# Kernel optimization log

Measured on AMD Instinct MI355X. Metric: run time of the kernel, lower is better.

## Reference

```python
import jax, jax.numpy as jnp
import numpy as np


def setup_inputs() -> dict:
    key = jax.random.key(0)
    ks = jax.random.split(key, 9)
    B, T, L, H2, E, V, OOV = 32, 48, 400, 512, 128, 50000, 100
    sd = lambda k, shape, s: jax.random.normal(k, shape, jnp.float32) * s
    return {
        "dec_hiddens": sd(ks[0], (B, T, H2), 1.0),   # decoder hidden state per step (B,T,2H)
        "enc_hiddens": sd(ks[1], (B, L, H2), 1.0),   # encoder outputs (B,L,2H)
        "W_enc": sd(ks[2], (H2, H2), 0.002),          # encoder-attention bilinear
        "W_dec": sd(ks[3], (H2, H2), 0.002),          # intra-decoder-attention bilinear
        "W_proj": sd(ks[4], (3 * H2, E), 0.02),       # decode2proj (6H -> emb)
        "W_vocab": sd(ks[5], (E, V), 0.05),           # proj2vocab (emb -> V, tied to embedding)
        "w_ptr": sd(ks[6], (3 * H2,), 0.02),          # ptr_gen weight
        "b_ptr": jnp.zeros((1,), jnp.float32),        # ptr_gen bias
        "extend_vocab": jax.random.randint(ks[7], (B, L), 0, V + OOV),
        "num_oov": OOV,
    }


def reference(dec_hiddens, enc_hiddens, W_enc, W_dec, W_proj, W_vocab,
              w_ptr, b_ptr, extend_vocab, num_oov):
    B, T, H2 = dec_hiddens.shape
    L = enc_hiddens.shape[1]
    V = W_vocab.shape[1]
    Vext = V + num_oov  # static python int
    rows = jnp.arange(B)[:, None]
    steps = jnp.arange(T)
    dec_seq = jnp.swapaxes(dec_hiddens, 0, 1)  # (T,B,2H) for scan

    def step(acc_exp, xs):
        h, t = xs  # h: (B,2H), t: scalar step index
        # intra-temporal encoder attention: exp(e) / running sum of previous exp(e)
        e = jnp.einsum('bh,hk,blk->bl', h, W_enc, enc_hiddens)  # (B,L)
        exp_e = jnp.exp(e)
        denom = jnp.where(t == 0, jnp.ones_like(acc_exp), acc_exp)
        temporal = exp_e / denom
        enc_att = temporal / temporal.sum(-1, keepdims=True)     # (B,L)
        enc_ctx = jnp.einsum('bl,blh->bh', enc_att, enc_hiddens)
        # intra-decoder attention over previous decoder hiddens (zeros at t=0)
        s = jnp.einsum('bh,hk,btk->bt', h, W_dec, dec_hiddens)   # (B,T)
        s = jnp.where((steps < t)[None, :], s, -1e30)
        datt = jax.nn.softmax(s, axis=-1)
        dec_ctx = jnp.where(t == 0, 0.0,
                            jnp.einsum('bt,bth->bh', datt, dec_hiddens))
        cat = jnp.concatenate([h, enc_ctx, dec_ctx], axis=-1)    # (B,6H)
        p = jax.nn.sigmoid(cat @ w_ptr + b_ptr)[:, None]         # (B,1) copy gate
        vocab_dist = jax.nn.softmax((cat @ W_proj) @ W_vocab, axis=-1)  # (B,V)
        # extended-vocab distribution: write softmax slice, scatter_add pointer dist
        final = jnp.zeros((B, Vext), dec_hiddens.dtype)
        final = final.at[:, :V].set((1.0 - p) * vocab_dist)
        final = final.at[rows, extend_vocab].add(p * enc_att)
        return acc_exp + exp_e, final

    init = jnp.zeros((B, L), dec_hiddens.dtype)
    _, out = jax.lax.scan(step, init, (dec_seq, steps))
    return jnp.swapaxes(out, 0, 1)  # (B,T,V+OOV)
```

## Files before the change

### kernel.cpp

```cpp
#include <hip/hip_runtime.h>
#include <hip/hip_bf16.h>
#include <cstdint>

typedef __attribute__((ext_vector_type(8))) short short8;
typedef __attribute__((ext_vector_type(4))) float floatx4;
typedef __attribute__((ext_vector_type(16))) float floatx16;

#define Bdim 32
#define Tdim 48
#define Ldim 400
#define Hdim 512
#define Edim 128
#define Vdim 50000
#define VEdim 50100
#define BTdim 1536
#define CATdim 1536
#define NPAD 50048
#define MTILES 96
#define NPART 782
#define NPSTRIDE 800

__device__ __forceinline__ short f2bf(float x){
    __hip_bfloat16 h = __float2bfloat16(x);
    union { __hip_bfloat16 h; short s; } u; u.h = h; return u.s;
}

__device__ __forceinline__ void gemm_nn_body(
    const float* __restrict__ A, int lda,
    const float* __restrict__ B, int ldb,
    float* __restrict__ C, int ldc,
    int M, int N, int K, int m0, int n0)
{
    __shared__ float As[16][68];
    __shared__ float Bs[16][68];
    const int tid = threadIdx.x;
    const int tx = tid & 15, ty = tid >> 4;
    const int ar = tid >> 2, ac = (tid & 3) * 4;
    const int br = tid >> 4, bc = (tid & 15) * 4;
    float acc[4][4] = {};
    float4 va = make_float4(0.f,0.f,0.f,0.f);
    float4 vb = make_float4(0.f,0.f,0.f,0.f);
    if (m0 + ar < M) va = *(const float4*)(A + (size_t)(m0+ar)*lda + ac);
    if (n0 + bc < N) vb = *(const float4*)(B + (size_t)br*ldb + n0 + bc);
    for (int k0 = 0; k0 < K; k0 += 16){
        As[ac+0][ar]=va.x; As[ac+1][ar]=va.y; As[ac+2][ar]=va.z; As[ac+3][ar]=va.w;
        Bs[br][bc+0]=vb.x; Bs[br][bc+1]=vb.y; Bs[br][bc+2]=vb.z; Bs[br][bc+3]=vb.w;
        __syncthreads();
        const int kn = k0 + 16;
        if (kn < K){
            va = make_float4(0.f,0.f,0.f,0.f);
            vb = make_float4(0.f,0.f,0.f,0.f);
            if (m0 + ar < M) va = *(const float4*)(A + (size_t)(m0+ar)*lda + kn + ac);
            if (n0 + bc < N) vb = *(const float4*)(B + (size_t)(kn+br)*ldb + n0 + bc);
        }
        #pragma unroll
        for (int k=0;k<16;k++){
            float a[4], b[4];
            #pragma unroll
            for (int i=0;i<4;i++) a[i] = As[k][ty*4+i];
            #pragma unroll
            for (int j=0;j<4;j++) b[j] = Bs[k][tx*4+j];
            #pragma unroll
            for (int i=0;i<4;i++)
                #pragma unroll
                for (int j=0;j<4;j++)
                    acc[i][j] += a[i]*b[j];
        }
        __syncthreads();
    }
    #pragma unroll
    for (int i=0;i<4;i++){
        int m = m0 + ty*4 + i;
        if (m >= M) continue;
        #pragma unroll
        for (int j=0;j<4;j++){
            int n = n0 + tx*4 + j;
            if (n < N) C[(size_t)m*ldc + n] = acc[i][j];
        }
    }
}

__device__ __forceinline__ void gemm_nt_body(
    const float* __restrict__ A, int lda,
    const float* __restrict__ B, int ldb,
    float* __restrict__ C, int ldc,
    int M, int N, int K, int m0, int n0)
{
    __shared__ float As[16][68];
    __shared__ float Bs[16][68];
    const int tid = threadIdx.x;
    const int tx = tid & 15, ty = tid >> 4;
    const int r = tid >> 2, c = (tid & 3) * 4;
    float acc[4][4] = {};
    float4 va = make_float4(0.f,0.f,0.f,0.f);
    float4 vb = make_float4(0.f,0.f,0.f,0.f);
    if (m0 + r < M) va = *(const float4*)(A + (size_t)(m0+r)*lda + c);
    if (n0 + r < N) vb = *(const float4*)(B + (size_t)(n0+r)*ldb + c);
    for (int k0 = 0; k0 < K; k0 += 16){
        As[c+0][r]=va.x; As[c+1][r]=va.y; As[c+2][r]=va.z; As[c+3][r]=va.w;
        Bs[c+0][r]=vb.x; Bs[c+1][r]=vb.y; Bs[c+2][r]=vb.z; Bs[c+3][r]=vb.w;
        __syncthreads();
        const int kn = k0 + 16;
        if (kn < K){
            va = make_float4(0.f,0.f,0.f,0.f);
            vb = make_float4(0.f,0.f,0.f,0.f);
            if (m0 + r < M) va = *(const float4*)(A + (size_t)(m0+r)*lda + kn + c);
            if (n0 + r < N) vb = *(const float4*)(B + (size_t)(n0+r)*ldb + kn + c);
        }
        #pragma unroll
        for (int k=0;k<16;k++){
            float a[4], b[4];
            #pragma unroll
            for (int i=0;i<4;i++) a[i] = As[k][ty*4+i];
            #pragma unroll
            for (int j=0;j<4;j++) b[j] = Bs[k][tx*4+j];
            #pragma unroll
            for (int i=0;i<4;i++)
                #pragma unroll
                for (int j=0;j<4;j++)
                    acc[i][j] += a[i]*b[j];
        }
        __syncthreads();
    }
    #pragma unroll
    for (int i=0;i<4;i++){
        int m = m0 + ty*4 + i;
        if (m >= M) continue;
        #pragma unroll
        for (int j=0;j<4;j++){
            int n = n0 + tx*4 + j;
            if (n < N) C[(size_t)m*ldc + n] = acc[i][j];
        }
    }
}

__global__ __launch_bounds__(256) void k_p12(
    const float* __restrict__ dec, const float* __restrict__ Wenc,
    const float* __restrict__ Wdec, float* __restrict__ P1, float* __restrict__ P2)
{
    const float* B = blockIdx.z ? Wdec : Wenc;
    float* C = blockIdx.z ? P2 : P1;
    gemm_nn_body(dec, Hdim, B, Hdim, C, Hdim, BTdim, Hdim, Hdim,
                 blockIdx.y*64, blockIdx.x*64);
}

__global__ __launch_bounds__(256) void k_es(
    const float* __restrict__ P1, const float* __restrict__ P2,
    const float* __restrict__ enc, const float* __restrict__ dec,
    float* __restrict__ ebuf, float* __restrict__ sbuf)
{
    int z = blockIdx.z;
    if (z < 32){
        gemm_nt_body(P1 + (size_t)z*Tdim*Hdim, Hdim,
                     enc + (size_t)z*Ldim*Hdim, Hdim,
                     ebuf + (size_t)z*Tdim*Ldim, Ldim,
                     Tdim, Ldim, Hdim, 0, blockIdx.x*64);
    } else {
        if (blockIdx.x) return;
        z -= 32;
        gemm_nt_body(P2 + (size_t)z*Tdim*Hdim, Hdim,
                     dec + (size_t)z*Tdim*Hdim, Hdim,
                     sbuf + (size_t)z*Tdim*Tdim, Tdim,
                     Tdim, Tdim, Hdim, 0, 0);
    }
}

__global__ __launch_bounds__(256) void k_tempdec(
    const float* __restrict__ e, float* __restrict__ att, float* __restrict__ sbuf)
{
    int bid = blockIdx.x;
    if (bid < 50){
        int idx = bid*256 + threadIdx.x;
        if (idx >= Bdim * Ldim) return;
        int b = idx / Ldim, l = idx % Ldim;
        const float* ep = e + (size_t)b * Tdim * Ldim + l;
        float* ap = att + (size_t)b * Tdim * Ldim + l;
        float acc = 0.f;
        for (int t = 0; t < Tdim; ++t){
            float x = __expf(ep[(size_t)t * Ldim]);
            float d = (t == 0) ? 1.f : acc;
            ap[(size_t)t * Ldim] = x / d;
            acc += x;
        }
    } else {
        int b = bid - 50;
        int t = threadIdx.x;
        if (t >= Tdim) return;
        float* row = sbuf + (size_t)b * Tdim * Tdim + (size_t)t * Tdim;
        if (t == 0){
            for (int j = 0; j < Tdim; ++j) row[j] = 0.f;
            return;
        }
        float mx = -1e30f;
        for (int j = 0; j < t; ++j) mx = fmaxf(mx, row[j]);
        float sum = 0.f;
        for (int j = 0; j < t; ++j){ float ex = __expf(row[j]-mx); row[j]=ex; sum+=ex; }
        float inv = 1.f/sum;
        for (int j = 0; j < t; ++j) row[j] *= inv;
        for (int j = t; j < Tdim; ++j) row[j] = 0.f;
    }
}

__global__ __launch_bounds__(256) void k_attnorm(float* __restrict__ att){
    int row = blockIdx.x;
    float* ap = att + (size_t)row * Ldim;
    float s = 0.f;
    for (int i = threadIdx.x; i < Ldim; i += 256) s += ap[i];
    #pragma unroll
    for (int off = 32; off; off >>= 1) s += __shfl_down(s, off, 64);
    __shared__ float red[4];
    if ((threadIdx.x & 63) == 0) red[threadIdx.x >> 6] = s;
    __syncthreads();
    float inv = 1.f / (red[0] + red[1] + red[2] + red[3]);
    for (int i = threadIdx.x; i < Ldim; i += 256) ap[i] *= inv;
}

__global__ __launch_bounds__(256) void k_ctx(
    const float* __restrict__ att, const float* __restrict__ sbuf,
    const float* __restrict__ enc, const float* __restrict__ dec,
    float* __restrict__ cat)
{
    int z = blockIdx.z;
    if (z >= 64){
        int idx = ((z-64)*8 + blockIdx.x)*256 + threadIdx.x;
        int m = idx >> 7, j = (idx & 127) << 2;
        *(float4*)(cat + (size_t)m*CATdim + j) =
            *(const float4*)(dec + (size_t)m*Hdim + j);
        return;
    }
    const float *A, *Bm; float* C; int lda, K;
    if (z < 32){
        A = att + (size_t)z*Tdim*Ldim; lda = Ldim;
        Bm = enc + (size_t)z*Ldim*Hdim;
        C = cat + (size_t)z*Tdim*CATdim + Hdim;
        K = Ldim;
    } else {
        int b = z - 32;
        A = sbuf + (size_t)b*Tdim*Tdim; lda = Tdim;
        Bm = dec + (size_t)b*Tdim*Hdim;
        C = cat + (size_t)b*Tdim*CATdim + 2*Hdim;
        K = Tdim;
    }
    gemm_nn_body(A, lda, Bm, Hdim, C, CATdim, Tdim, Hdim, K, 0, blockIdx.x*64);
}

__global__ __launch_bounds__(256) void k_proj(
    const float* __restrict__ cat, const float* __restrict__ Wproj,
    float* __restrict__ projf4)
{
    int z = blockIdx.z;
    gemm_nn_body(cat + (size_t)z*384, CATdim,
                 Wproj + (size_t)z*384*Edim, Edim,
                 projf4 + (size_t)z*BTdim*Edim, Edim,
                 BTdim, Edim, 384, blockIdx.y*64, blockIdx.x*64);
}

__global__ __launch_bounds__(256) void k_post(
    const float* __restrict__ cat, const float* __restrict__ wp,
    const float* __restrict__ bp, float* __restrict__ pg,
    const float* __restrict__ pf, short* __restrict__ pb,
    const float* __restrict__ Wv, short* __restrict__ Wt)
{
    __shared__ float smem[32*33];
    int bid = blockIdx.x;
    if (bid < BTdim){
        const float* cp = cat + (size_t)bid*CATdim;
        float s = 0.f;
        for (int i=threadIdx.x;i<CATdim;i+=256) s += cp[i]*wp[i];
        #pragma unroll
        for (int off=32; off; off>>=1) s += __shfl_down(s, off, 64);
        if ((threadIdx.x&63)==0) smem[threadIdx.x>>6]=s;
        __syncthreads();
        if (threadIdx.x==0){
            float tot = smem[0]+smem[1]+smem[2]+smem[3] + bp[0];
            pg[bid] = 1.f/(1.f + __expf(-tot));
        }
        return;
    }
    if (bid < BTdim + 768){
        int i = (bid - BTdim)*256 + threadIdx.x;
        pb[i] = f2bf(pf[i] + pf[i + 196608] + pf[i + 2*196608] + pf[i + 3*196608]);
        return;
    }
    int b2 = bid - (BTdim + 768);
    int n0 = (b2 % 1564)*32, k0 = (b2 / 1564)*32;
    float (*tile)[33] = reinterpret_cast<float(*)[33]>(smem);
    int x = threadIdx.x & 31, y0 = threadIdx.x >> 5;
    for (int yy=y0; yy<32; yy+=8){
        int n = n0 + x;
        tile[yy][x] = (n < Vdim) ? Wv[(size_t)(k0+yy)*Vdim + n] : 0.f;
    }
    __syncthreads();
    for (int yy=y0; yy<32; yy+=8){
        int n = n0 + yy;
        if (n < NPAD) Wt[(size_t)n*Edim + k0 + x] = f2bf(tile[x][yy]);
    }
}

__global__ __launch_bounds__(256) void k_logits1(
    const short* __restrict__ Ab, const short* __restrict__ Bt,
    float* __restrict__ partial)
{
    const int lane = threadIdx.x & 63;
    const int wave = threadIdx.x >> 6;
    const int l15 = lane & 15, quad = lane >> 4;
    const int wid = blockIdx.x*4 + wave;
    if (wid >= NPART) return;
    const int n0 = wid*64;
    short8 bfrag[4][4];
    #pragma unroll
    for (int ct=0;ct<4;ct++){
        const short* bp = Bt + (size_t)(n0 + ct*16 + l15)*Edim + quad*8;
        #pragma unroll
        for (int kk=0;kk<4;kk++) bfrag[ct][kk] = *(const short8*)(bp + kk*32);
    }
    float vmask[4];
    #pragma unroll
    for (int ct=0;ct<4;ct++) vmask[ct] = (n0 + ct*16 < Vdim) ? 1.f : 0.f;

    auto loadA = [&](int mt, short8 (&af)[4]){
        const short* ap = Ab + (size_t)(mt*16 + l15)*Edim + quad*8;
        #pragma unroll
        for (int kk=0;kk<4;kk++) af[kk] = *(const short8*)(ap + kk*32);
    };
    auto compute = [&](int mt, short8 (&af)[4]){
        floatx4 a0 = {0.f,0.f,0.f,0.f};
        floatx4 a1 = a0, a2 = a0, a3 = a0;
        #pragma unroll
        for (int kk=0;kk<4;kk++){
            a0 = __builtin_amdgcn_mfma_f32_16x16x32_bf16(bfrag[0][kk], af[kk], a0, 0, 0, 0);
            a1 = __builtin_amdgcn_mfma_f32_16x16x32_bf16(bfrag[1][kk], af[kk], a1, 0, 0, 0);
            a2 = __builtin_amdgcn_mfma_f32_16x16x32_bf16(bfrag[2][kk], af[kk], a2, 0, 0, 0);
            a3 = __builtin_amdgcn_mfma_f32_16x16x32_bf16(bfrag[3][kk], af[kk], a3, 0, 0, 0);
        }
        float s = vmask[0]*(__expf(a0[0])+__expf(a0[1])+__expf(a0[2])+__expf(a0[3]))
                + vmask[1]*(__expf(a1[0])+__expf(a1[1])+__expf(a1[2])+__expf(a1[3]))
                + vmask[2]*(__expf(a2[0])+__expf(a2[1])+__expf(a2[2])+__expf(a2[3]))
                + vmask[3]*(__expf(a3[0])+__expf(a3[1])+__expf(a3[2])+__expf(a3[3]));
        s += __shfl_xor(s, 16, 64);
        s += __shfl_xor(s, 32, 64);
        if (lane < 16)
            partial[(size_t)(mt*16 + l15)*NPSTRIDE + wid] = s;
    };

    short8 afA[4], afB[4];
    loadA(0, afA);
    for (int mt=0; mt<MTILES; mt+=2){
        loadA(mt+1, afB);
        compute(mt, afA);
        if (mt+2 < MTILES) loadA(mt+2, afA);
        compute(mt+1, afB);
    }
}

__global__ __launch_bounds__(256) void k_reduce(const float* __restrict__ partial,
                         const float* __restrict__ pg, float* __restrict__ scale){
    int m = blockIdx.x;
    float s = 0.f;
    for (int w = threadIdx.x; w < NPART; w += 256)
        s += partial[(size_t)m*NPSTRIDE + w];
    #pragma unroll
    for (int off=32; off; off>>=1) s += __shfl_down(s, off, 64);
    __shared__ float red[4];
    if ((threadIdx.x&63)==0) red[threadIdx.x>>6]=s;
    __syncthreads();
    if (threadIdx.x==0)
        scale[m] = (1.f - pg[m]) / (red[0]+red[1]+red[2]+red[3]);
}

__global__ __launch_bounds__(256) void k_logits2(
    const short* __restrict__ Ab, const short* __restrict__ Bt,
    const float* __restrict__ scale, float* __restrict__ out)
{
    const int lane = threadIdx.x & 63;
    const int wave = threadIdx.x >> 6;
    const int l31 = lane & 31, half = lane >> 5;
    const int n0 = blockIdx.x*128 + wave*32;
    const int n = n0 + l31;
    const int mt0 = blockIdx.y * 24;
    if (n0 >= Vdim){
        if (n < VEdim){
            for (int mt=mt0; mt<mt0+24; ++mt){
                #pragma unroll
                for (int r=0;r<16;r++){
                    int m = mt*32 + (r&3) + 8*(r>>2) + 4*half;
                    out[(size_t)m*VEdim + n] = 0.f;
                }
            }
        }
        return;
    }
    short8 bfrag[8];
    const short* bp = Bt + (size_t)n*Edim + half*8;
    #pragma unroll
    for (int kk=0;kk<8;kk++) bfrag[kk] = *(const short8*)(bp + kk*16);
    const bool valid = n < Vdim;
    for (int mt=mt0; mt<mt0+24; ++mt){
        floatx16 acc;
        #pragma unroll
        for (int i=0;i<16;i++) acc[i] = 0.f;
        const short* ap = Ab + (size_t)(mt*32 + l31)*Edim + half*8;
        #pragma unroll
        for (int kk=0;kk<8;kk++){
            short8 af = *(const short8*)(ap + kk*16);
            acc = __builtin_amdgcn_mfma_f32_32x32x16_bf16(af, bfrag[kk], acc, 0, 0, 0);
        }
        #pragma unroll
        for (int r=0;r<16;r++){
            int m = mt*32 + (r&3) + 8*(r>>2) + 4*half;
            if (valid) out[(size_t)m*VEdim + n] = scale[m]*__expf(acc[r]);
            else if (n < VEdim) out[(size_t)m*VEdim + n] = 0.f;
        }
    }
}

__global__ void k_scatter(const float* __restrict__ att, const float* __restrict__ pg,
                          const int* __restrict__ ev, float* __restrict__ out){
    int idx = blockIdx.x*256 + threadIdx.x;
    if (idx >= BTdim*Ldim) return;
    int m = idx / Ldim, l = idx % Ldim;
    int b = m / Tdim;
    int v = ev[b*Ldim + l];
    atomicAdd(&out[(size_t)m*VEdim + v], pg[m]*att[idx]);
}

extern "C" void kernel_launch(void* const* d_in, const int* in_sizes, int n_in,
                              void* d_out, int out_size, void* d_ws, size_t ws_size,
                              hipStream_t stream)
{
    const float* dec  = (const float*)d_in[0];
    const float* enc  = (const float*)d_in[1];
    const float* Wenc = (const float*)d_in[2];
    const float* Wdec = (const float*)d_in[3];
    const float* Wproj= (const float*)d_in[4];
    const float* Wvoc = (const float*)d_in[5];
    const float* wptr = (const float*)d_in[6];
    const float* bptr = (const float*)d_in[7];
    const int*   ev   = (const int*)d_in[8];
    float* out = (float*)d_out;

    float* ws = (float*)d_ws;
    float* P1      = ws;
    float* P2      = P1 + 786432;
    float* ebuf    = P2 + 786432;
    float* att     = ebuf + 614400;
    float* sbuf    = att + 614400;
    float* cat     = sbuf + 73728;
    float* projf4  = cat + 2359296;
    float* pg      = projf4 + 4*196608;
    float* scale   = pg + 1536;
    float* partial = scale + 1536;
    short* projb   = (short*)(partial + (size_t)BTdim*NPSTRIDE);
    short* Wt      = projb + 196608;

    dim3 blk(256);
    k_p12<<<dim3(8,24,2), blk, 0, stream>>>(dec, Wenc, Wdec, P1, P2);
    k_es<<<dim3(7,1,64), blk, 0, stream>>>(P1, P2, enc, dec, ebuf, sbuf);
    k_tempdec<<<dim3(82), blk, 0, stream>>>(ebuf, att, sbuf);
    k_attnorm<<<dim3(BTdim), blk, 0, stream>>>(att);
    k_ctx<<<dim3(8,1,160), blk, 0, stream>>>(att, sbuf, enc, dec, cat);
    k_proj<<<dim3(2,24,4), blk, 0, stream>>>(cat, Wproj, projf4);
    k_post<<<dim3(BTdim + 768 + 6256), blk, 0, stream>>>(cat, wptr, bptr, pg,
                                                         projf4, projb, Wvoc, Wt);
    k_logits1<<<dim3(196), blk, 0, stream>>>(projb, Wt, partial);
    k_reduce<<<dim3(BTdim), blk, 0, stream>>>(partial, pg, scale);
    k_logits2<<<dim3(392,2), blk, 0, stream>>>(projb, Wt, scale, out);
    k_scatter<<<dim3((BTdim*Ldim+255)/256), blk, 0, stream>>>(att, pg, ev, out);
}
```

Measured before the change: 704.4 us.

## Fuse pipeline into seven kernels with algebraic pointer gate and fused scatter

Collapses eleven launches into seven. The P1/P2 GEMMs, the W_vocab transpose, the cat copy and the precomputed enc/dec dot products with w_ptr all go into one grid. The pointer gate is now computed algebraically from attention-weighted projections (att·(enc·w2)) instead of a full dot over cat, and temporal attention, its normalisation and the decoder softmax are fused into one per-batch kernel. The projection GEMM runs K=1536 without split-K and writes bf16 directly. The logits partial sums go through atomics instead of a separate reduce kernel. The scatter is folded into the logits-write kernel by bucketing hits per column block. The trade-offs are less parallelism in the kE projection (48 blocks) and kC (32 blocks), plus a large LDS footprint in kC.

```diff
diff --git a/kernel.cpp b/kernel.cpp
--- a/kernel.cpp
+++ b/kernel.cpp
@@ -18,21 +18,26 @@
 #define NPAD 50048
 #define MTILES 96
 #define NPART 782
-#define NPSTRIDE 800
 
 __device__ __forceinline__ short f2bf(float x){
     __hip_bfloat16 h = __float2bfloat16(x);
     union { __hip_bfloat16 h; short s; } u; u.h = h; return u.s;
 }
 
+__device__ __forceinline__ float wred(float s){
+    #pragma unroll
+    for (int off = 32; off; off >>= 1) s += __shfl_xor(s, off, 64);
+    return s;
+}
+
+template<bool BF16>
 __device__ __forceinline__ void gemm_nn_body(
     const float* __restrict__ A, int lda,
     const float* __restrict__ B, int ldb,
-    float* __restrict__ C, int ldc,
-    int M, int N, int K, int m0, int n0)
-{
-    __shared__ float As[16][68];
-    __shared__ float Bs[16][68];
+    float* __restrict__ C, short* __restrict__ Cb, int ldc,
+    int M, int N, int K, int m0, int n0,
+    float (*As)[68], float (*Bs)[68])
+{
     const int tid = threadIdx.x;
     const int tx = tid & 15, ty = tid >> 4;
     const int ar = tid >> 2, ac = (tid & 3) * 4;
@@ -75,7 +80,10 @@
         #pragma unroll
         for (int j=0;j<4;j++){
             int n = n0 + tx*4 + j;
-            if (n < N) C[(size_t)m*ldc + n] = acc[i][j];
+            if (n < N){
+                if (BF16) Cb[(size_t)m*ldc + n] = f2bf(acc[i][j]);
+                else      C[(size_t)m*ldc + n]  = acc[i][j];
+            }
         }
     }
 }
@@ -84,10 +92,9 @@
     const float* __restrict__ A, int lda,
     const float* __restrict__ B, int ldb,
     float* __restrict__ C, int ldc,
-    int M, int N, int K, int m0, int n0)
-{
-    __shared__ float As[16][68];
-    __shared__ float Bs[16][68];
+    int M, int N, int K, int m0, int n0,
+    float (*As)[68], float (*Bs)[68])
+{
     const int tid = threadIdx.x;
     const int tx = tid & 15, ty = tid >> 4;
     const int r = tid >> 2, c = (tid & 3) * 4;
@@ -134,172 +141,209 @@
     }
 }
 
-__global__ __launch_bounds__(256) void k_p12(
+__global__ __launch_bounds__(256) void kA(
     const float* __restrict__ dec, const float* __restrict__ Wenc,
-    const float* __restrict__ Wdec, float* __restrict__ P1, float* __restrict__ P2)
-{
-    const float* B = blockIdx.z ? Wdec : Wenc;
-    float* C = blockIdx.z ? P2 : P1;
-    gemm_nn_body(dec, Hdim, B, Hdim, C, Hdim, BTdim, Hdim, Hdim,
-                 blockIdx.y*64, blockIdx.x*64);
-}
-
-__global__ __launch_bounds__(256) void k_es(
-    const float* __restrict__ P1, const float* __restrict__ P2,
-    const float* __restrict__ enc, const float* __restrict__ dec,
-    float* __restrict__ ebuf, float* __restrict__ sbuf)
-{
-    int z = blockIdx.z;
-    if (z < 32){
-        gemm_nt_body(P1 + (size_t)z*Tdim*Hdim, Hdim,
-                     enc + (size_t)z*Ldim*Hdim, Hdim,
-                     ebuf + (size_t)z*Tdim*Ldim, Ldim,
-                     Tdim, Ldim, Hdim, 0, blockIdx.x*64);
-    } else {
-        if (blockIdx.x) return;
-        z -= 32;
-        gemm_nt_body(P2 + (size_t)z*Tdim*Hdim, Hdim,
-                     dec + (size_t)z*Tdim*Hdim, Hdim,
-                     sbuf + (size_t)z*Tdim*Tdim, Tdim,
-                     Tdim, Tdim, Hdim, 0, 0);
-    }
-}
-
-__global__ __launch_bounds__(256) void k_tempdec(
-    const float* __restrict__ e, float* __restrict__ att, float* __restrict__ sbuf)
-{
+    const float* __restrict__ Wdec, float* __restrict__ P1, float* __restrict__ P2,
+    float* __restrict__ cat,
+    const float* __restrict__ Wv, short* __restrict__ Wt,
+    const float* __restrict__ enc, const float* __restrict__ wptr,
+    float* __restrict__ q_enc, float* __restrict__ q_dec,
+    float* __restrict__ sums)
+{
+    __shared__ float As[16][68];
+    __shared__ float Bs[16][68];
     int bid = blockIdx.x;
-    if (bid < 50){
+    if (bid < 384){
+        int z = bid / 192, r = bid % 192;
+        gemm_nn_body<false>(dec, Hdim, z ? Wdec : Wenc, Hdim,
+                            z ? P2 : P1, nullptr, Hdim,
+                            BTdim, Hdim, Hdim, (r>>3)*64, (r&7)*64, As, Bs);
+        return;
+    }
+    bid -= 384;
+    if (bid < 768){
         int idx = bid*256 + threadIdx.x;
-        if (idx >= Bdim * Ldim) return;
-        int b = idx / Ldim, l = idx % Ldim;
-        const float* ep = e + (size_t)b * Tdim * Ldim + l;
-        float* ap = att + (size_t)b * Tdim * Ldim + l;
-        float acc = 0.f;
-        for (int t = 0; t < Tdim; ++t){
-            float x = __expf(ep[(size_t)t * Ldim]);
-            float d = (t == 0) ? 1.f : acc;
-            ap[(size_t)t * Ldim] = x / d;
-            acc += x;
-        }
-    } else {
-        int b = bid - 50;
-        int t = threadIdx.x;
-        if (t >= Tdim) return;
-        float* row = sbuf + (size_t)b * Tdim * Tdim + (size_t)t * Tdim;
-        if (t == 0){
-            for (int j = 0; j < Tdim; ++j) row[j] = 0.f;
-            return;
-        }
-        float mx = -1e30f;
-        for (int j = 0; j < t; ++j) mx = fmaxf(mx, row[j]);
-        float sum = 0.f;
-        for (int j = 0; j < t; ++j){ float ex = __expf(row[j]-mx); row[j]=ex; sum+=ex; }
-        float inv = 1.f/sum;
-        for (int j = 0; j < t; ++j) row[j] *= inv;
-        for (int j = t; j < Tdim; ++j) row[j] = 0.f;
-    }
-}
-
-__global__ __launch_bounds__(256) void k_attnorm(float* __restrict__ att){
-    int row = blockIdx.x;
-    float* ap = att + (size_t)row * Ldim;
-    float s = 0.f;
-    for (int i = threadIdx.x; i < Ldim; i += 256) s += ap[i];
-    #pragma unroll
-    for (int off = 32; off; off >>= 1) s += __shfl_down(s, off, 64);
-    __shared__ float red[4];
-    if ((threadIdx.x & 63) == 0) red[threadIdx.x >> 6] = s;
-    __syncthreads();
-    float inv = 1.f / (red[0] + red[1] + red[2] + red[3]);
-    for (int i = threadIdx.x; i < Ldim; i += 256) ap[i] *= inv;
-}
-
-__global__ __launch_bounds__(256) void k_ctx(
-    const float* __restrict__ att, const float* __restrict__ sbuf,
-    const float* __restrict__ enc, const float* __restrict__ dec,
-    float* __restrict__ cat)
-{
-    int z = blockIdx.z;
-    if (z >= 64){
-        int idx = ((z-64)*8 + blockIdx.x)*256 + threadIdx.x;
         int m = idx >> 7, j = (idx & 127) << 2;
         *(float4*)(cat + (size_t)m*CATdim + j) =
             *(const float4*)(dec + (size_t)m*Hdim + j);
         return;
     }
-    const float *A, *Bm; float* C; int lda, K;
-    if (z < 32){
-        A = att + (size_t)z*Tdim*Ldim; lda = Ldim;
-        Bm = enc + (size_t)z*Ldim*Hdim;
-        C = cat + (size_t)z*Tdim*CATdim + Hdim;
-        K = Ldim;
+    bid -= 768;
+    if (bid < 6256){
+        float (*tile)[33] = reinterpret_cast<float(*)[33]>(&As[0][0]);
+        int n0 = (bid % 1564)*32, k0 = (bid / 1564)*32;
+        int x = threadIdx.x & 31, y0 = threadIdx.x >> 5;
+        for (int yy=y0; yy<32; yy+=8){
+            int n = n0 + x;
+            tile[yy][x] = (n < Vdim) ? Wv[(size_t)(k0+yy)*Vdim + n] : 0.f;
+        }
+        __syncthreads();
+        for (int yy=y0; yy<32; yy+=8){
+            int n = n0 + yy;
+            if (n < NPAD) Wt[(size_t)n*Edim + k0 + x] = f2bf(tile[x][yy]);
+        }
+        return;
+    }
+    bid -= 6256;
+    if (bid < 128){
+        int b = bid >> 2, part = bid & 3;
+        int wv = threadIdx.x >> 6, lane = threadIdx.x & 63;
+        const float* w2 = wptr + Hdim;
+        const float* w3 = wptr + 2*Hdim;
+        for (int r = part*100 + wv; r < part*100 + 100; r += 4){
+            const float* rp = enc + ((size_t)b*Ldim + r)*Hdim;
+            float s = 0.f;
+            #pragma unroll
+            for (int i = 0; i < 8; i++) s += rp[lane + i*64]*w2[lane + i*64];
+            s = wred(s);
+            if (lane == 0) q_enc[b*Ldim + r] = s;
+        }
+        if (part == 0){
+            for (int r = wv; r < Tdim; r += 4){
+                const float* rp = dec + ((size_t)b*Tdim + r)*Hdim;
+                float s = 0.f;
+                #pragma unroll
+                for (int i = 0; i < 8; i++) s += rp[lane + i*64]*w3[lane + i*64];
+                s = wred(s);
+                if (lane == 0) q_dec[b*Tdim + r] = s;
+            }
+        }
+        return;
+    }
+    for (int i = threadIdx.x; i < BTdim; i += 256) sums[i] = 0.f;
+}
+
+__global__ __launch_bounds__(256) void kB(
+    const float* __restrict__ P1, const float* __restrict__ P2,
+    const float* __restrict__ enc, const float* __restrict__ dec,
+    float* __restrict__ ebuf, float* __restrict__ sbuf)
+{
+    __shared__ float As[16][68];
+    __shared__ float Bs[16][68];
+    int bid = blockIdx.x;
+    if (bid < 224){
+        int z = bid / 7, x = bid % 7;
+        gemm_nt_body(P1 + (size_t)z*Tdim*Hdim, Hdim,
+                     enc + (size_t)z*Ldim*Hdim, Hdim,
+                     ebuf + (size_t)z*Tdim*Ldim, Ldim,
+                     Tdim, Ldim, Hdim, 0, x*64, As, Bs);
     } else {
-        int b = z - 32;
-        A = sbuf + (size_t)b*Tdim*Tdim; lda = Tdim;
-        Bm = dec + (size_t)b*Tdim*Hdim;
-        C = cat + (size_t)b*Tdim*CATdim + 2*Hdim;
-        K = Tdim;
-    }
-    gemm_nn_body(A, lda, Bm, Hdim, C, CATdim, Tdim, Hdim, K, 0, blockIdx.x*64);
-}
-
-__global__ __launch_bounds__(256) void k_proj(
+        int z = bid - 224;
+        gemm_nt_body(P2 + (size_t)z*Tdim*Hdim, Hdim,
+                     dec + (size_t)z*Tdim*Hdim, Hdim,
+                     sbuf + (size_t)z*Tdim*Tdim, Tdim,
+                     Tdim, Tdim, Hdim, 0, 0, As, Bs);
+    }
+}
+
+__global__ __launch_bounds__(512) void kC(
+    const float* __restrict__ e, float* __restrict__ att, float* __restrict__ sbuf,
+    const float* __restrict__ dec, const float* __restrict__ wptr,
+    const float* __restrict__ bptr,
+    const float* __restrict__ q_enc, const float* __restrict__ q_dec,
+    float* __restrict__ pg)
+{
+    __shared__ float att_s[Tdim][Ldim];
+    __shared__ float dE[Tdim], dD[Tdim], dH[Tdim];
+    const int b = blockIdx.x;
+    const int tid = threadIdx.x;
+    if (tid < Ldim){
+        const float* ep = e + (size_t)b*Tdim*Ldim + tid;
+        float acc = 0.f;
+        for (int t = 0; t < Tdim; ++t){
+            float x = __expf(ep[t*Ldim]);
+            att_s[t][tid] = x / (t ? acc : 1.f);
+            acc += x;
+        }
+    }
+    __syncthreads();
+    const int wv = tid >> 6, lane = tid & 63;
+    for (int t = wv; t < Tdim; t += 8){
+        float s1 = 0.f, s2 = 0.f;
+        for (int l = lane; l < Ldim; l += 64){
+            float a = att_s[t][l];
+            s1 += a;
+            s2 += a * q_enc[b*Ldim + l];
+        }
+        s1 = wred(s1); s2 = wred(s2);
+        float inv = 1.f/s1;
+        if (lane == 0) dE[t] = s2*inv;
+        for (int l = lane; l < Ldim; l += 64)
+            att[(size_t)(b*Tdim + t)*Ldim + l] = att_s[t][l]*inv;
+    }
+    for (int t = wv; t < Tdim; t += 8){
+        const float* hp = dec + ((size_t)b*Tdim + t)*Hdim;
+        float s = 0.f;
+        #pragma unroll
+        for (int i = 0; i < 8; i++) s += hp[lane + i*64]*wptr[lane + i*64];
+        s = wred(s);
+        if (lane == 0) dH[t] = s;
+    }
+    for (int t = wv; t < Tdim; t += 8){
+        float* row = sbuf + ((size_t)b*Tdim + t)*Tdim;
+        if (t == 0){
+            if (lane < Tdim) row[lane] = 0.f;
+            if (lane == 0) dD[0] = 0.f;
+        } else {
+            float v = (lane < t) ? row[lane] : -1e30f;
+            float mx = v;
+            #pragma unroll
+            for (int off = 32; off; off >>= 1) mx = fmaxf(mx, __shfl_xor(mx, off, 64));
+            float ex = (lane < t) ? __expf(v - mx) : 0.f;
+            float sm = wred(ex);
+            float nv = ex / sm;
+            if (lane < Tdim) row[lane] = nv;
+            float d = (lane < Tdim) ? nv * q_dec[b*Tdim + lane] : 0.f;
+            d = wred(d);
+            if (lane == 0) dD[t] = d;
+        }
+    }
+    __syncthreads();
+    if (tid < Tdim){
+        float tot = dH[tid] + dE[tid] + dD[tid] + bptr[0];
+        pg[b*Tdim + tid] = 1.f/(1.f + __expf(-tot));
+    }
+}
+
+__global__ __launch_bounds__(256) void kD(
+    const float* __restrict__ att, const float* __restrict__ sbuf,
+    const float* __restrict__ enc, const float* __restrict__ dec,
+    float* __restrict__ cat)
+{
+    __shared__ float As[16][68];
+    __shared__ float Bs[16][68];
+    int bid = blockIdx.x;
+    if (bid < 256){
+        int z = bid >> 3, x = bid & 7;
+        gemm_nn_body<false>(att + (size_t)z*Tdim*Ldim, Ldim,
+                            enc + (size_t)z*Ldim*Hdim, Hdim,
+                            cat + (size_t)z*Tdim*CATdim + Hdim, nullptr, CATdim,
+                            Tdim, Hdim, Ldim, 0, x*64, As, Bs);
+    } else {
+        int r = bid - 256;
+        int z = r >> 3, x = r & 7;
+        gemm_nn_body<false>(sbuf + (size_t)z*Tdim*Tdim, Tdim,
+                            dec + (size_t)z*Tdim*Hdim, Hdim,
+                            cat + (size_t)z*Tdim*CATdim + 2*Hdim, nullptr, CATdim,
+                            Tdim, Hdim, Tdim, 0, x*64, As, Bs);
+    }
+}
+
+__global__ __launch_bounds__(256) void kE(
     const float* __restrict__ cat, const float* __restrict__ Wproj,
-    float* __restrict__ projf4)
-{
-    int z = blockIdx.z;
-    gemm_nn_body(cat + (size_t)z*384, CATdim,
-                 Wproj + (size_t)z*384*Edim, Edim,
-                 projf4 + (size_t)z*BTdim*Edim, Edim,
-                 BTdim, Edim, 384, blockIdx.y*64, blockIdx.x*64);
-}
-
-__global__ __launch_bounds__(256) void k_post(
-    const float* __restrict__ cat, const float* __restrict__ wp,
-    const float* __restrict__ bp, float* __restrict__ pg,
-    const float* __restrict__ pf, short* __restrict__ pb,
-    const float* __restrict__ Wv, short* __restrict__ Wt)
-{
-    __shared__ float smem[32*33];
-    int bid = blockIdx.x;
-    if (bid < BTdim){
-        const float* cp = cat + (size_t)bid*CATdim;
-        float s = 0.f;
-        for (int i=threadIdx.x;i<CATdim;i+=256) s += cp[i]*wp[i];
-        #pragma unroll
-        for (int off=32; off; off>>=1) s += __shfl_down(s, off, 64);
-        if ((threadIdx.x&63)==0) smem[threadIdx.x>>6]=s;
-        __syncthreads();
-        if (threadIdx.x==0){
-            float tot = smem[0]+smem[1]+smem[2]+smem[3] + bp[0];
-            pg[bid] = 1.f/(1.f + __expf(-tot));
-        }
-        return;
-    }
-    if (bid < BTdim + 768){
-        int i = (bid - BTdim)*256 + threadIdx.x;
-        pb[i] = f2bf(pf[i] + pf[i + 196608] + pf[i + 2*196608] + pf[i + 3*196608]);
-        return;
-    }
-    int b2 = bid - (BTdim + 768);
-    int n0 = (b2 % 1564)*32, k0 = (b2 / 1564)*32;
-    float (*tile)[33] = reinterpret_cast<float(*)[33]>(smem);
-    int x = threadIdx.x & 31, y0 = threadIdx.x >> 5;
-    for (int yy=y0; yy<32; yy+=8){
-        int n = n0 + x;
-        tile[yy][x] = (n < Vdim) ? Wv[(size_t)(k0+yy)*Vdim + n] : 0.f;
-    }
-    __syncthreads();
-    for (int yy=y0; yy<32; yy+=8){
-        int n = n0 + yy;
-        if (n < NPAD) Wt[(size_t)n*Edim + k0 + x] = f2bf(tile[x][yy]);
-    }
-}
-
-__global__ __launch_bounds__(256) void k_logits1(
+    short* __restrict__ projb)
+{
+    __shared__ float As[16][68];
+    __shared__ float Bs[16][68];
+    int by = blockIdx.x >> 1, bx = blockIdx.x & 1;
+    gemm_nn_body<true>(cat, CATdim, Wproj, Edim,
+                       nullptr, projb, Edim,
+                       BTdim, Edim, CATdim, by*64, bx*64, As, Bs);
+}
+
+__global__ __launch_bounds__(256) void kF(
     const short* __restrict__ Ab, const short* __restrict__ Bt,
-    float* __restrict__ partial)
+    float* __restrict__ sums)
 {
     const int lane = threadIdx.x & 63;
     const int wave = threadIdx.x >> 6;
@@ -340,44 +384,43 @@
         s += __shfl_xor(s, 16, 64);
         s += __shfl_xor(s, 32, 64);
         if (lane < 16)
-            partial[(size_t)(mt*16 + l15)*NPSTRIDE + wid] = s;
+            atomicAdd(&sums[mt*16 + l15], s);
     };
 
+    const int mt0 = blockIdx.y*48, mt1 = mt0 + 48;
     short8 afA[4], afB[4];
-    loadA(0, afA);
-    for (int mt=0; mt<MTILES; mt+=2){
+    loadA(mt0, afA);
+    for (int mt=mt0; mt<mt1; mt+=2){
         loadA(mt+1, afB);
         compute(mt, afA);
-        if (mt+2 < MTILES) loadA(mt+2, afA);
+        if (mt+2 < mt1) loadA(mt+2, afA);
         compute(mt+1, afB);
     }
 }
 
-__global__ __launch_bounds__(256) void k_reduce(const float* __restrict__ partial,
-                         const float* __restrict__ pg, float* __restrict__ scale){
-    int m = blockIdx.x;
-    float s = 0.f;
-    for (int w = threadIdx.x; w < NPART; w += 256)
-        s += partial[(size_t)m*NPSTRIDE + w];
-    #pragma unroll
-    for (int off=32; off; off>>=1) s += __shfl_down(s, off, 64);
-    __shared__ float red[4];
-    if ((threadIdx.x&63)==0) red[threadIdx.x>>6]=s;
-    __syncthreads();
-    if (threadIdx.x==0)
-        scale[m] = (1.f - pg[m]) / (red[0]+red[1]+red[2]+red[3]);
-}
-
-__global__ __launch_bounds__(256) void k_logits2(
+__global__ __launch_bounds__(256) void kG(
     const short* __restrict__ Ab, const short* __restrict__ Bt,
-    const float* __restrict__ scale, float* __restrict__ out)
-{
+    const float* __restrict__ sums, const float* __restrict__ pg,
+    const float* __restrict__ att, const int* __restrict__ ev,
+    float* __restrict__ out)
+{
+    __shared__ float scl[768];
+    __shared__ int hits[6400];
+    __shared__ int hcnt;
     const int lane = threadIdx.x & 63;
     const int wave = threadIdx.x >> 6;
     const int l31 = lane & 31, half = lane >> 5;
     const int n0 = blockIdx.x*128 + wave*32;
     const int n = n0 + l31;
-    const int mt0 = blockIdx.y * 24;
+    const int yoff = blockIdx.y*768;
+    const int mt0 = blockIdx.y*24;
+    for (int i = threadIdx.x; i < 768; i += 256){
+        int m = yoff + i;
+        scl[i] = (1.f - pg[m]) / sums[m];
+    }
+    if (threadIdx.x == 0) hcnt = 0;
+    __syncthreads();
+
     if (n0 >= Vdim){
         if (n < VEdim){
             for (int mt=mt0; mt<mt0+24; ++mt){
@@ -388,40 +431,50 @@
                 }
             }
         }
-        return;
-    }
-    short8 bfrag[8];
-    const short* bp = Bt + (size_t)n*Edim + half*8;
-    #pragma unroll
-    for (int kk=0;kk<8;kk++) bfrag[kk] = *(const short8*)(bp + kk*16);
-    const bool valid = n < Vdim;
-    for (int mt=mt0; mt<mt0+24; ++mt){
-        floatx16 acc;
-        #pragma unroll
-        for (int i=0;i<16;i++) acc[i] = 0.f;
-        const short* ap = Ab + (size_t)(mt*32 + l31)*Edim + half*8;
-        #pragma unroll
-        for (int kk=0;kk<8;kk++){
-            short8 af = *(const short8*)(ap + kk*16);
-            acc = __builtin_amdgcn_mfma_f32_32x32x16_bf16(af, bfrag[kk], acc, 0, 0, 0);
-        }
-        #pragma unroll
-        for (int r=0;r<16;r++){
-            int m = mt*32 + (r&3) + 8*(r>>2) + 4*half;
-            if (valid) out[(size_t)m*VEdim + n] = scale[m]*__expf(acc[r]);
-            else if (n < VEdim) out[(size_t)m*VEdim + n] = 0.f;
-        }
-    }
-}
-
-__global__ void k_scatter(const float* __restrict__ att, const float* __restrict__ pg,
-                          const int* __restrict__ ev, float* __restrict__ out){
-    int idx = blockIdx.x*256 + threadIdx.x;
-    if (idx >= BTdim*Ldim) return;
-    int m = idx / Ldim, l = idx % Ldim;
-    int b = m / Tdim;
-    int v = ev[b*Ldim + l];
-    atomicAdd(&out[(size_t)m*VEdim + v], pg[m]*att[idx]);
+    } else {
+        short8 bfrag[8];
+        const short* bp = Bt + (size_t)n*Edim + half*8;
+        #pragma unroll
+        for (int kk=0;kk<8;kk++) bfrag[kk] = *(const short8*)(bp + kk*16);
+        const bool valid = n < Vdim;
+        for (int mt=mt0; mt<mt0+24; ++mt){
+            floatx16 acc;
+            #pragma unroll
+            for (int i=0;i<16;i++) acc[i] = 0.f;
+            const short* ap = Ab + (size_t)(mt*32 + l31)*Edim + half*8;
+            #pragma unroll
+            for (int kk=0;kk<8;kk++){
+                short8 af = *(const short8*)(ap + kk*16);
+                acc = __builtin_amdgcn_mfma_f32_32x32x16_bf16(af, bfrag[kk], acc, 0, 0, 0);
+            }
+            #pragma unroll
+            for (int r=0;r<16;r++){
+                int m = mt*32 + (r&3) + 8*(r>>2) + 4*half;
+                if (valid) out[(size_t)m*VEdim + n] = scl[m - yoff]*__expf(acc[r]);
+                else if (n < VEdim) out[(size_t)m*VEdim + n] = 0.f;
+            }
+        }
+    }
+    for (int idx = threadIdx.x; idx < 16*Ldim; idx += 256){
+        int b = (blockIdx.y << 4) + idx/Ldim;
+        int l = idx % Ldim;
+        int v = ev[b*Ldim + l];
+        if ((v >> 7) == (int)blockIdx.x){
+            int h = atomicAdd(&hcnt, 1);
+            hits[h] = (v << 14) | ((b & 31) << 9) | l;
+        }
+    }
+    __syncthreads();
+    const int tot = hcnt * Tdim;
+    for (int j = threadIdx.x; j < tot; j += 256){
+        int h = j / Tdim, t = j % Tdim;
+        int pk = hits[h];
+        int v = pk >> 14;
+        int b = (pk >> 9) & 31;
+        int l = pk & 511;
+        int m = b*Tdim + t;
+        atomicAdd(&out[(size_t)m*VEdim + v], pg[m]*att[(size_t)m*Ldim + l]);
+    }
 }
 
 extern "C" void kernel_launch(void* const* d_in, const int* in_sizes, int n_in,
@@ -440,30 +493,27 @@
     float* out = (float*)d_out;
 
     float* ws = (float*)d_ws;
-    float* P1      = ws;
-    float* P2      = P1 + 786432;
-    float* ebuf    = P2 + 786432;
-    float* att     = ebuf + 614400;
-    float* sbuf    = att + 614400;
-    float* cat     = sbuf + 73728;
-    float* projf4  = cat + 2359296;
-    float* pg      = projf4 + 4*196608;
-    float* scale   = pg + 1536;
-    float* partial = scale + 1536;
-    short* projb   = (short*)(partial + (size_t)BTdim*NPSTRIDE);
-    short* Wt      = projb + 196608;
+    float* P1    = ws;
+    float* P2    = P1 + 786432;
+    float* ebuf  = P2 + 786432;
+    float* att   = ebuf + 614400;
+    float* sbuf  = att + 614400;
+    float* cat   = sbuf + 73728;
+    float* q_enc = cat + 2359296;
+    float* q_dec = q_enc + 12800;
+    float* pg    = q_dec + 1536;
+    float* sums  = pg + 1536;
+    short* projb = (short*)(sums + 1536);
+    short* Wt    = projb + 196608;
 
     dim3 blk(256);
-    k_p12<<<dim3(8,24,2), blk, 0, stream>>>(dec, Wenc, Wdec, P1, P2);
-    k_es<<<dim3(7,1,64), blk, 0, stream>>>(P1, P2, enc, dec, ebuf, sbuf);
-    k_tempdec<<<dim3(82), blk, 0, stream>>>(ebuf, att, sbuf);
-    k_attnorm<<<dim3(BTdim), blk, 0, stream>>>(att);
-    k_ctx<<<dim3(8,1,160), blk, 0, stream>>>(att, sbuf, enc, dec, cat);
-    k_proj<<<dim3(2,24,4), blk, 0, stream>>>(cat, Wproj, projf4);
-    k_post<<<dim3(BTdim + 768 + 6256), blk, 0, stream>>>(cat, wptr, bptr, pg,
-                                                         projf4, projb, Wvoc, Wt);
-    k_logits1<<<dim3(196), blk, 0, stream>>>(projb, Wt, partial);
-    k_reduce<<<dim3(BTdim), blk, 0, stream>>>(partial, pg, scale);
-    k_logits2<<<dim3(392,2), blk, 0, stream>>>(projb, Wt, scale, out);
-    k_scatter<<<dim3((BTdim*Ldim+255)/256), blk, 0, stream>>>(att, pg, ev, out);
-}
+    kA<<<dim3(7537), blk, 0, stream>>>(dec, Wenc, Wdec, P1, P2, cat,
+                                       Wvoc, Wt, enc, wptr, q_enc, q_dec, sums);
+    kB<<<dim3(256), blk, 0, stream>>>(P1, P2, enc, dec, ebuf, sbuf);
+    kC<<<dim3(Bdim), dim3(512), 0, stream>>>(ebuf, att, sbuf, dec, wptr, bptr,
+                                             q_enc, q_dec, pg);
+    kD<<<dim3(512), blk, 0, stream>>>(att, sbuf, enc, dec, cat);
+    kE<<<dim3(48), blk, 0, stream>>>(cat, Wproj, projb);
+    kF<<<dim3(196,2), blk, 0, stream>>>(projb, Wt, sums);
+    kG<<<dim3(392,2), blk, 0, stream>>>(projb, Wt, sums, pg, att, ev, out);
+}
```

Result: slower. 746.9 us (+6.0%).
